# Optimization experiments

Measured on AMD Instinct MI355X. Metric: run time of the kernel, lower is better.

Reference implementation:

```python
import jax, jax.numpy as jnp
import numpy as np

NUM_HEAD = 16
FEAT_DIM = 1024
HEAD_DIM = FEAT_DIM // NUM_HEAD  # 64
MAX_SEQ_LEN = 2048
BATCH = 2


def setup_inputs() -> dict:
    key = jax.random.key(0)
    ks = jax.random.split(key, 6)
    x = jax.random.normal(ks[0], (BATCH, MAX_SEQ_LEN, FEAT_DIM), dtype=jnp.float32)
    # xavier_uniform: limit = sqrt(6/(fan_in+fan_out)); torch Linear weight is [out, in]
    def xavier(k, out_f, in_f):
        lim = float(np.sqrt(6.0 / (in_f + out_f)))
        return jax.random.uniform(k, (out_f, in_f), dtype=jnp.float32, minval=-lim, maxval=lim)
    W1 = xavier(ks[1], HEAD_DIM, HEAD_DIM)          # attn_mlp[0].weight
    b1 = jnp.zeros((HEAD_DIM,), dtype=jnp.float32)
    W2 = xavier(ks[2], MAX_SEQ_LEN, HEAD_DIM)       # attn_mlp[2].weight
    b2 = jnp.zeros((MAX_SEQ_LEN,), dtype=jnp.float32)
    Wv = xavier(ks[3], FEAT_DIM, FEAT_DIM)          # value_linear.weight (no bias)
    Wo = xavier(ks[4], FEAT_DIM, FEAT_DIM)          # output_linear.weight (no bias)
    return {"x": x, "W1": W1, "b1": b1, "W2": W2, "b2": b2, "Wv": Wv, "Wo": Wo}


def _split_head(t):
    b, n, _ = t.shape
    return t.reshape(b, n, NUM_HEAD, HEAD_DIM).transpose(0, 2, 1, 3)  # [b,h,n,d]


def reference(x, W1, b1, W2, b2, Wv, Wo):
    # value projection (dropout is identity in eval / p=0)
    value = x @ Wv.T                                   # [b,n,F]
    vh = _split_head(value)                            # [b,h,n,d]
    xh = _split_head(x)                                # [b,h,n,d]
    # per-head MLP -> dense attention logits [b,h,n,max_seq_len]
    hid = jax.nn.relu(jnp.einsum('bhnd,ed->bhne', xh, W1) + b1)
    logits = jnp.einsum('bhne,me->bhnm', hid, W2) + b2
    attn = jax.nn.softmax(logits, axis=-1)             # [b,h,n,m]
    out_h = jnp.einsum('bhnm,bhmd->bhnd', attn, vh)    # m == seq_len
    b_, h_, n_, d_ = out_h.shape
    out = out_h.transpose(0, 2, 1, 3).reshape(b_, n_, FEAT_DIM)
    return out @ Wo.T
```

## Files before the change

### kernel.cpp

```cpp
#include <hip/hip_runtime.h>
#include <hip/hip_bf16.h>
#include <math.h>
#include <stdint.h>


typedef __attribute__((ext_vector_type(8))) short bf16x8;
typedef __attribute__((ext_vector_type(4))) float f32x4;
typedef __attribute__((ext_vector_type(16))) float f32x16;

#define LOG2E 1.4426950408889634f

__device__ __forceinline__ unsigned short f2bf(float f) {
  union { float f; unsigned u; } v; v.f = f;
  unsigned r = v.u + 0x7FFFu + ((v.u >> 16) & 1u);
  return (unsigned short)(r >> 16);
}

__global__ __launch_bounds__(256) void prep_all(const float* __restrict__ x,
                                                const float* __restrict__ Wv,
                                                const float* __restrict__ Wo,
                                                const float* __restrict__ W2,
                                                const float* __restrict__ W1,
                                                const float* __restrict__ b2,
                                                unsigned short* __restrict__ xb,
                                                unsigned short* __restrict__ wvb,
                                                unsigned short* __restrict__ wob,
                                                unsigned short* __restrict__ w2b,
                                                unsigned short* __restrict__ w1b,
                                                float* __restrict__ b2l) {
  int bid = blockIdx.x;
  if (bid == 2048) {
    int i = threadIdx.x;
#pragma unroll
    for (int t = 0; t < 8; ++t) {
      int k = i * 8 + t;
      b2l[k] = b2[k] * LOG2E;
    }
    return;
  }
  int stride = 2048 * 256;
  for (int q = bid * 256 + threadIdx.x; q < 1606656; q += stride) {
    const float* s; unsigned short* d; int o;
    if (q < 1048576)      { s = x;  d = xb;  o = q; }
    else {
      int q2 = q - 1048576;
      if (q2 < 262144)      { s = Wv; d = wvb; o = q2; }
      else if (q2 < 524288) { s = Wo; d = wob; o = q2 - 262144; }
      else if (q2 < 557056) { s = W2; d = w2b; o = q2 - 524288; }
      else                  { s = W1; d = w1b; o = q2 - 557056; }
    }
    float4 v = *(const float4*)(s + (size_t)o * 4);
    uint2 u;
    u.x = (unsigned)f2bf(v.x) | ((unsigned)f2bf(v.y) << 16);
    u.y = (unsigned)f2bf(v.z) | ((unsigned)f2bf(v.w) << 16);
    *(uint2*)(d + (size_t)o * 4) = u;
  }
}

__device__ __forceinline__ void stage64(const char* g, size_t ldbytes, char* lds,
                                        int w, int lane) {
#pragma unroll
  for (int t = 0; t < 2; ++t) {
    int row  = w * 16 + t * 8 + (lane >> 3);
    int csrc = (lane & 7) ^ (lane >> 3);
    const char* src = g + (size_t)row * ldbytes + (csrc << 4);
    char* dst = lds + ((w * 2 + t) << 10);
    __builtin_amdgcn_global_load_lds((const __attribute__((address_space(1))) void*)src,
                                     (__attribute__((address_space(3))) void*)dst,
                                     16, 0, 0);
  }
}

__device__ __forceinline__ void stage8(const char* g, size_t ldbytes, char* lds_,
                                       int w, int lane) {
  int row  = w * 8 + (lane >> 3);
  int csrc = (lane & 7) ^ (lane >> 3);
  const char* src = g + (size_t)row * ldbytes + (csrc << 4);
  char* dst = lds_ + (w << 10);
  __builtin_amdgcn_global_load_lds((const __attribute__((address_space(1))) void*)src,
                                   (__attribute__((address_space(3))) void*)dst,
                                   16, 0, 0);
}

__device__ __forceinline__ bf16x8 rdfrag32(const char* lds, int row, int chunk) {
  int c = chunk ^ (row & 7);
  return *(const bf16x8*)(lds + row * 128 + (c << 4));
}

__device__ __forceinline__ f32x16 loadb16(const float* p) {
  f32x16 r;
#pragma unroll
  for (int qd = 0; qd < 4; ++qd) {
    float4 v = *(const float4*)(p + qd * 8);
    r[qd * 4 + 0] = v.x; r[qd * 4 + 1] = v.y; r[qd * 4 + 2] = v.z; r[qd * 4 + 3] = v.w;
  }
  return r;
}

__device__ __forceinline__ bf16x8 pk_swap(float r0, float r1, float r2, float r3,
                                          float r4, float r5, float r6, float r7) {
  unsigned a, b, c, d;
  asm("v_cvt_pk_bf16_f32 %0, %1, %2" : "=v"(a) : "v"(r0), "v"(r1));
  asm("v_cvt_pk_bf16_f32 %0, %1, %2" : "=v"(b) : "v"(r4), "v"(r5));
  asm("v_cvt_pk_bf16_f32 %0, %1, %2" : "=v"(c) : "v"(r2), "v"(r3));
  asm("v_cvt_pk_bf16_f32 %0, %1, %2" : "=v"(d) : "v"(r6), "v"(r7));
  asm("v_permlane32_swap_b32 %0, %1" : "+v"(a), "+v"(b));
  asm("v_permlane32_swap_b32 %0, %1" : "+v"(c), "+v"(d));
  union { unsigned u[4]; bf16x8 v; } r;
  r.u[0] = a; r.u[1] = c; r.u[2] = b; r.u[3] = d;
  return r.v;
}

template<int MODE>
__global__ __launch_bounds__(256) void gemm12864(const unsigned short* __restrict__ A,
                                                 const unsigned short* __restrict__ B,
                                                 void* __restrict__ C, int K) {
  __shared__ __attribute__((aligned(16))) char As[2][16384];
  __shared__ __attribute__((aligned(16))) char Bs[2][8192];
  int tid = threadIdx.x, w = tid >> 6, lane = tid & 63;
  int l31 = lane & 31, hi = lane >> 5;
  int wr = w >> 1, wc = w & 1;
  int bm = blockIdx.x, bn = blockIdx.y;
  const char* Ab = (const char*)A + (size_t)bm * 128 * (K * 2);
  const char* Bb = (const char*)B + (size_t)bn * 64 * (K * 2);
  size_t ld = (size_t)K * 2;

  f32x16 acc0 = {}, acc1 = {};
  stage64(Ab, ld, As[0], w, lane);
  stage64(Ab + 64 * ld, ld, As[0] + 8192, w, lane);
  stage64(Bb, ld, Bs[0], w, lane);
  __syncthreads();

  int nst = K >> 6;
  for (int kk = 0; kk < nst; ++kk) {
    int cur = kk & 1;
    if (kk + 1 < nst) {
      const char* An = Ab + (size_t)(kk + 1) * 128;
      const char* Bn = Bb + (size_t)(kk + 1) * 128;
      stage64(An, ld, As[cur ^ 1], w, lane);
      stage64(An + 64 * ld, ld, As[cur ^ 1] + 8192, w, lane);
      stage64(Bn, ld, Bs[cur ^ 1], w, lane);
    }
    __builtin_amdgcn_s_setprio(1);
#pragma unroll
    for (int ks = 0; ks < 4; ++ks) {
      bf16x8 a0 = rdfrag32(As[cur], wr * 64 + l31, ks * 2 + hi);
      bf16x8 a1 = rdfrag32(As[cur], wr * 64 + 32 + l31, ks * 2 + hi);
      bf16x8 b0 = rdfrag32(Bs[cur], wc * 32 + l31, ks * 2 + hi);
      acc0 = __builtin_amdgcn_mfma_f32_32x32x16_bf16(a0, b0, acc0, 0, 0, 0);
      acc1 = __builtin_amdgcn_mfma_f32_32x32x16_bf16(a1, b0, acc1, 0, 0, 0);
    }
    __builtin_amdgcn_s_setprio(0);
    __syncthreads();
  }

  if (MODE == 0) {
    unsigned short* vt = (unsigned short*)C;
    int d = wc * 32 + l31;
#pragma unroll
    for (int i = 0; i < 2; ++i) {
      f32x16 a = i ? acc1 : acc0;
      int rowb = bm * 128 + wr * 64 + i * 32;
#pragma unroll
      for (int qd = 0; qd < 4; ++qd) {
        int m0 = rowb + qd * 8 + hi * 4;
        int bb = m0 >> 11, n = m0 & 2047;
        int r0 = qd * 4;
        uint2 u;
        u.x = (unsigned)f2bf(a[r0]) | ((unsigned)f2bf(a[r0 + 1]) << 16);
        u.y = (unsigned)f2bf(a[r0 + 2]) | ((unsigned)f2bf(a[r0 + 3]) << 16);
        *(uint2*)(vt + ((size_t)((bb * 16 + bn) * 64 + d)) * 2048 + n) = u;
      }
    }
  } else {
    float* Cf = (float*)C;
    int rb = bm * 128 + wr * 64, cb = bn * 64 + wc * 32;
#pragma unroll
    for (int r = 0; r < 16; ++r) {
      int row = (r & 3) + 8 * (r >> 2) + 4 * hi;
      Cf[(size_t)(rb + row) * 1024 + cb + l31]      = acc0[r];
      Cf[(size_t)(rb + 32 + row) * 1024 + cb + l31] = acc1[r];
    }
  }
}

__global__ __launch_bounds__(512, 2) void flash_kernel(const unsigned short* __restrict__ xb,
                                                       const unsigned short* __restrict__ w1b,
                                                       const float* __restrict__ b1,
                                                       const unsigned short* __restrict__ w2b,
                                                       const float* __restrict__ b2l,
                                                       const unsigned short* __restrict__ vt,
                                                       unsigned short* __restrict__ aout) {
  __shared__ __attribute__((aligned(16))) char lds[73728];
  int tid = threadIdx.x, w = tid >> 6, lane = tid & 63;
  int wq = w & 3, grp = w >> 2;
  int l31 = lane & 31, hi = lane >> 5;
  int f = blockIdx.x;
  int swz = ((f & 7) << 6) | (f >> 3);
  int qt = swz & 15, bh = swz >> 4;
  int b = bh >> 4, h = bh & 15;

  const char* px = (const char*)(xb + ((size_t)(b * 2048 + qt * 128)) * 1024 + h * 64);
  stage8(px, 2048, lds, w, lane);
  stage8(px + (size_t)64 * 2048, 2048, lds + 8192, w, lane);
  stage8((const char*)w1b, 128, lds + 32768, w, lane);
  {
    const char* src = (const char*)b2l + (w << 10) + (lane << 4);
    char* dst = lds + 65536 + (w << 10);
    __builtin_amdgcn_global_load_lds((const __attribute__((address_space(1))) void*)src,
                                     (__attribute__((address_space(3))) void*)dst,
                                     16, 0, 0);
  }
  __syncthreads();

  f32x16 h0 = loadb16(b1 + hi * 4);
  f32x16 h1 = loadb16(b1 + 32 + hi * 4);
  {
    const char* xt = lds + (wq >> 1) * 8192;
    int xr = (wq & 1) * 32 + l31;
#pragma unroll
    for (int ks = 0; ks < 4; ++ks) {
      bf16x8 xf = rdfrag32(xt, xr, ks * 2 + hi);
      bf16x8 wf0 = rdfrag32(lds + 32768, l31, ks * 2 + hi);
      h0 = __builtin_amdgcn_mfma_f32_32x32x16_bf16(wf0, xf, h0, 0, 0, 0);
      bf16x8 wf1 = rdfrag32(lds + 32768, 32 + l31, ks * 2 + hi);
      h1 = __builtin_amdgcn_mfma_f32_32x32x16_bf16(wf1, xf, h1, 0, 0, 0);
    }
  }
#pragma unroll
  for (int i = 0; i < 16; ++i) {
    h0[i] = fmaxf(h0[i], 0.f) * LOG2E;
    h1[i] = fmaxf(h1[i], 0.f) * LOG2E;
  }
  bf16x8 qb[4];
  qb[0] = pk_swap(h0[0], h0[1], h0[2], h0[3], h0[4], h0[5], h0[6], h0[7]);
  qb[1] = pk_swap(h0[8], h0[9], h0[10], h0[11], h0[12], h0[13], h0[14], h0[15]);
  qb[2] = pk_swap(h1[0], h1[1], h1[2], h1[3], h1[4], h1[5], h1[6], h1[7]);
  qb[3] = pk_swap(h1[8], h1[9], h1[10], h1[11], h1[12], h1[13], h1[14], h1[15]);
  __syncthreads();

  const char* vtb = (const char*)vt + (size_t)bh * 64 * 4096;
#pragma unroll
  for (int t = 0; t < 4; ++t) {
    stage8((const char*)w2b + (size_t)t * 8192, 128, lds + t * 8192, w, lane);
    stage8(vtb + (size_t)t * 128, 4096, lds + 32768 + t * 8192, w, lane);
  }
  bf16x8 ones;
#pragma unroll
  for (int i = 0; i < 8; ++i) ones[i] = (short)0x3F80;
  f32x16 oA = {}, oB = {}, Lac = {};
  const float* bl = (const float*)(lds + 65536);
  __syncthreads();

  for (int s = 0; s < 16; ++s) {
    int mt = 2 * s + grp;
    const char* Kc = lds + (mt & 3) * 8192;
    const char* Vc = lds + 32768 + (mt & 3) * 8192;

    if (s >= 1 && s <= 14) {
      int t0 = 2 * s + 2, t1 = 2 * s + 3;
      stage8((const char*)w2b + (size_t)t0 * 8192, 128, lds + (t0 & 3) * 8192, w, lane);
      stage8(vtb + (size_t)t0 * 128, 4096, lds + 32768 + (t0 & 3) * 8192, w, lane);
      stage8((const char*)w2b + (size_t)t1 * 8192, 128, lds + (t1 & 3) * 8192, w, lane);
      stage8(vtb + (size_t)t1 * 128, 4096, lds + 32768 + (t1 & 3) * 8192, w, lane);
    }

    f32x16 s0, s1;
#pragma unroll
    for (int qd = 0; qd < 4; ++qd) {
      f32x4 p0 = *(const f32x4*)(bl + mt * 64 + qd * 8 + hi * 4);
      f32x4 p1 = *(const f32x4*)(bl + mt * 64 + 32 + qd * 8 + hi * 4);
#pragma unroll
      for (int j = 0; j < 4; ++j) {
        s0[qd * 4 + j] = p0[j];
        s1[qd * 4 + j] = p1[j];
      }
    }
    __builtin_amdgcn_s_setprio(1);
#pragma unroll
    for (int kt = 0; kt < 4; ++kt) {
      bf16x8 kf0 = rdfrag32(Kc, l31, kt * 2 + hi);
      s0 = __builtin_amdgcn_mfma_f32_32x32x16_bf16(kf0, qb[kt], s0, 0, 0, 0);
      bf16x8 kf1 = rdfrag32(Kc, 32 + l31, kt * 2 + hi);
      s1 = __builtin_amdgcn_mfma_f32_32x32x16_bf16(kf1, qb[kt], s1, 0, 0, 0);
    }
    __builtin_amdgcn_s_setprio(0);
#pragma unroll
    for (int i = 0; i < 16; ++i) {
      float t0, t1;
      asm("v_exp_f32 %0, %1" : "=v"(t0) : "v"(s0[i]));
      asm("v_exp_f32 %0, %1" : "=v"(t1) : "v"(s1[i]));
      s0[i] = t0; s1[i] = t1;
    }
    bf16x8 pa0 = pk_swap(s0[0], s0[1], s0[2], s0[3], s0[4], s0[5], s0[6], s0[7]);
    bf16x8 pa1 = pk_swap(s0[8], s0[9], s0[10], s0[11], s0[12], s0[13], s0[14], s0[15]);
    bf16x8 pa2 = pk_swap(s1[0], s1[1], s1[2], s1[3], s1[4], s1[5], s1[6], s1[7]);
    bf16x8 pa3 = pk_swap(s1[8], s1[9], s1[10], s1[11], s1[12], s1[13], s1[14], s1[15]);
    __builtin_amdgcn_s_setprio(1);
    Lac = __builtin_amdgcn_mfma_f32_32x32x16_bf16(pa0, ones, Lac, 0, 0, 0);
    Lac = __builtin_amdgcn_mfma_f32_32x32x16_bf16(pa1, ones, Lac, 0, 0, 0);
    Lac = __builtin_amdgcn_mfma_f32_32x32x16_bf16(pa2, ones, Lac, 0, 0, 0);
    Lac = __builtin_amdgcn_mfma_f32_32x32x16_bf16(pa3, ones, Lac, 0, 0, 0);
    {
      bf16x8 vf;
      vf = rdfrag32(Vc, l31, 0 + hi);
      oA = __builtin_amdgcn_mfma_f32_32x32x16_bf16(pa0, vf, oA, 0, 0, 0);
      vf = rdfrag32(Vc, 32 + l31, 0 + hi);
      oB = __builtin_amdgcn_mfma_f32_32x32x16_bf16(pa0, vf, oB, 0, 0, 0);
      vf = rdfrag32(Vc, l31, 2 + hi);
      oA = __builtin_amdgcn_mfma_f32_32x32x16_bf16(pa1, vf, oA, 0, 0, 0);
      vf = rdfrag32(Vc, 32 + l31, 2 + hi);
      oB = __builtin_amdgcn_mfma_f32_32x32x16_bf16(pa1, vf, oB, 0, 0, 0);
      vf = rdfrag32(Vc, l31, 4 + hi);
      oA = __builtin_amdgcn_mfma_f32_32x32x16_bf16(pa2, vf, oA, 0, 0, 0);
      vf = rdfrag32(Vc, 32 + l31, 4 + hi);
      oB = __builtin_amdgcn_mfma_f32_32x32x16_bf16(pa2, vf, oB, 0, 0, 0);
      vf = rdfrag32(Vc, l31, 6 + hi);
      oA = __builtin_amdgcn_mfma_f32_32x32x16_bf16(pa3, vf, oA, 0, 0, 0);
      vf = rdfrag32(Vc, 32 + l31, 6 + hi);
      oB = __builtin_amdgcn_mfma_f32_32x32x16_bf16(pa3, vf, oB, 0, 0, 0);
    }
    __builtin_amdgcn_s_setprio(0);
    __syncthreads();
  }

  float* comb = (float*)lds;
  if (grp == 1) {
    float* cb = comb + (wq * 64 + lane) * 52;
#pragma unroll
    for (int i = 0; i < 4; ++i) {
      *(float4*)(cb + i * 4)      = make_float4(oA[i*4], oA[i*4+1], oA[i*4+2], oA[i*4+3]);
      *(float4*)(cb + 16 + i * 4) = make_float4(oB[i*4], oB[i*4+1], oB[i*4+2], oB[i*4+3]);
      *(float4*)(cb + 32 + i * 4) = make_float4(Lac[i*4], Lac[i*4+1], Lac[i*4+2], Lac[i*4+3]);
    }
  }
  __syncthreads();
  if (grp == 0) {
    float* cb = comb + (wq * 64 + lane) * 52;
#pragma unroll
    for (int i = 0; i < 4; ++i) {
      float4 a = *(const float4*)(cb + i * 4);
      float4 bq = *(const float4*)(cb + 16 + i * 4);
      float4 c = *(const float4*)(cb + 32 + i * 4);
      oA[i*4] += a.x;  oA[i*4+1] += a.y;  oA[i*4+2] += a.z;  oA[i*4+3] += a.w;
      oB[i*4] += bq.x; oB[i*4+1] += bq.y; oB[i*4+2] += bq.z; oB[i*4+3] += bq.w;
      Lac[i*4] += c.x; Lac[i*4+1] += c.y; Lac[i*4+2] += c.z; Lac[i*4+3] += c.w;
    }
    int nb = qt * 128 + wq * 32;
#pragma unroll
    for (int r = 0; r < 16; ++r) {
      float iv = 1.f / Lac[r];
      int ql = (r & 3) + 8 * (r >> 2) + 4 * hi;
      size_t off = ((size_t)(b * 2048 + nb + ql)) * 1024 + h * 64 + l31;
      aout[off]      = f2bf(oA[r] * iv);
      aout[off + 32] = f2bf(oB[r] * iv);
    }
  }
}

extern "C" void kernel_launch(void* const* d_in, const int* in_sizes, int n_in,
                              void* d_out, int out_size, void* d_ws, size_t ws_size,
                              hipStream_t stream) {
  (void)in_sizes; (void)n_in; (void)out_size; (void)ws_size;
  const float* x  = (const float*)d_in[0];
  const float* W1 = (const float*)d_in[1];
  const float* b1 = (const float*)d_in[2];
  const float* W2 = (const float*)d_in[3];
  const float* b2 = (const float*)d_in[4];
  const float* Wv = (const float*)d_in[5];
  const float* Wo = (const float*)d_in[6];
  float* out = (float*)d_out;

  char* ws = (char*)d_ws;
  unsigned short* xb   = (unsigned short*)(ws);
  unsigned short* wvb  = (unsigned short*)(ws +  8388608);
  unsigned short* wob  = (unsigned short*)(ws + 10485760);
  unsigned short* w2b  = (unsigned short*)(ws + 12582912);
  unsigned short* w1b  = (unsigned short*)(ws + 12845056);
  float*          b2l  = (float*)         (ws + 12853248);
  unsigned short* vt   = (unsigned short*)(ws + 21233664);
  unsigned short* aout = (unsigned short*)(ws + 29622272);

  prep_all<<<2049, 256, 0, stream>>>(x, Wv, Wo, W2, W1, b2,
                                     xb, wvb, wob, w2b, w1b, b2l);

  gemm12864<0><<<dim3(32, 16), 256, 0, stream>>>(xb, wvb, (void*)vt, 1024);
  flash_kernel<<<512, 512, 0, stream>>>(xb, w1b, b1, w2b, b2l, vt, aout);
  gemm12864<1><<<dim3(32, 16), 256, 0, stream>>>(aout, wob, (void*)out, 1024);
}
```

Before: 92.28 us.

## Fold exp(b2) into V and row-sum weights, switch bf16 to fp16 MFMA

The bias b2 is moved out of the logits: exp(b2) is folded into the value projection output and into the B operand of the row-sum MFMA. This removes the per-tile bias LDS load and staging and shrinks LDS. All operands switch from bf16 to fp16 with round-toward-zero packing. This risks overflow or precision issues if values exceed the fp16 range, and it assumes b2 is bounded.

```diff
diff --git a/kernel.cpp b/kernel.cpp
--- a/kernel.cpp
+++ b/kernel.cpp
@@ -4,16 +4,17 @@
 #include <stdint.h>
 
 
-typedef __attribute__((ext_vector_type(8))) short bf16x8;
+typedef __attribute__((ext_vector_type(8))) _Float16 f16x8;
+typedef __attribute__((ext_vector_type(2))) __fp16 h2;
 typedef __attribute__((ext_vector_type(4))) float f32x4;
 typedef __attribute__((ext_vector_type(16))) float f32x16;
 
 #define LOG2E 1.4426950408889634f
 
-__device__ __forceinline__ unsigned short f2bf(float f) {
-  union { float f; unsigned u; } v; v.f = f;
-  unsigned r = v.u + 0x7FFFu + ((v.u >> 16) & 1u);
-  return (unsigned short)(r >> 16);
+__device__ __forceinline__ unsigned short f2h(float f) {
+  union { _Float16 h; unsigned short u; } v;
+  v.h = (_Float16)f;
+  return v.u;
 }
 
 __global__ __launch_bounds__(256) void prep_all(const float* __restrict__ x,
@@ -27,14 +28,17 @@
                                                 unsigned short* __restrict__ wob,
                                                 unsigned short* __restrict__ w2b,
                                                 unsigned short* __restrict__ w1b,
-                                                float* __restrict__ b2l) {
+                                                float* __restrict__ eb2f,
+                                                unsigned short* __restrict__ ebb) {
   int bid = blockIdx.x;
   if (bid == 2048) {
     int i = threadIdx.x;
 #pragma unroll
     for (int t = 0; t < 8; ++t) {
       int k = i * 8 + t;
-      b2l[k] = b2[k] * LOG2E;
+      float e = __expf(b2[k]);
+      eb2f[k] = e;
+      ebb[k] = f2h(e);
     }
     return;
   }
@@ -51,8 +55,8 @@
     }
     float4 v = *(const float4*)(s + (size_t)o * 4);
     uint2 u;
-    u.x = (unsigned)f2bf(v.x) | ((unsigned)f2bf(v.y) << 16);
-    u.y = (unsigned)f2bf(v.z) | ((unsigned)f2bf(v.w) << 16);
+    u.x = (unsigned)f2h(v.x) | ((unsigned)f2h(v.y) << 16);
+    u.y = (unsigned)f2h(v.z) | ((unsigned)f2h(v.w) << 16);
     *(uint2*)(d + (size_t)o * 4) = u;
   }
 }
@@ -82,9 +86,9 @@
                                    16, 0, 0);
 }
 
-__device__ __forceinline__ bf16x8 rdfrag32(const char* lds, int row, int chunk) {
+__device__ __forceinline__ f16x8 rdfrag32(const char* lds, int row, int chunk) {
   int c = chunk ^ (row & 7);
-  return *(const bf16x8*)(lds + row * 128 + (c << 4));
+  return *(const f16x8*)(lds + row * 128 + (c << 4));
 }
 
 __device__ __forceinline__ f32x16 loadb16(const float* p) {
@@ -97,24 +101,25 @@
   return r;
 }
 
-__device__ __forceinline__ bf16x8 pk_swap(float r0, float r1, float r2, float r3,
-                                          float r4, float r5, float r6, float r7) {
-  unsigned a, b, c, d;
-  asm("v_cvt_pk_bf16_f32 %0, %1, %2" : "=v"(a) : "v"(r0), "v"(r1));
-  asm("v_cvt_pk_bf16_f32 %0, %1, %2" : "=v"(b) : "v"(r4), "v"(r5));
-  asm("v_cvt_pk_bf16_f32 %0, %1, %2" : "=v"(c) : "v"(r2), "v"(r3));
-  asm("v_cvt_pk_bf16_f32 %0, %1, %2" : "=v"(d) : "v"(r6), "v"(r7));
-  asm("v_permlane32_swap_b32 %0, %1" : "+v"(a), "+v"(b));
-  asm("v_permlane32_swap_b32 %0, %1" : "+v"(c), "+v"(d));
-  union { unsigned u[4]; bf16x8 v; } r;
-  r.u[0] = a; r.u[1] = c; r.u[2] = b; r.u[3] = d;
+__device__ __forceinline__ f16x8 pk_swap(float r0, float r1, float r2, float r3,
+                                         float r4, float r5, float r6, float r7) {
+  union { h2 h; unsigned u; } a, b, c, d;
+  a.h = __builtin_amdgcn_cvt_pkrtz(r0, r1);
+  b.h = __builtin_amdgcn_cvt_pkrtz(r4, r5);
+  c.h = __builtin_amdgcn_cvt_pkrtz(r2, r3);
+  d.h = __builtin_amdgcn_cvt_pkrtz(r6, r7);
+  asm("v_permlane32_swap_b32 %0, %1" : "+v"(a.u), "+v"(b.u));
+  asm("v_permlane32_swap_b32 %0, %1" : "+v"(c.u), "+v"(d.u));
+  union { unsigned u[4]; f16x8 v; } r;
+  r.u[0] = a.u; r.u[1] = c.u; r.u[2] = b.u; r.u[3] = d.u;
   return r.v;
 }
 
 template<int MODE>
 __global__ __launch_bounds__(256) void gemm12864(const unsigned short* __restrict__ A,
                                                  const unsigned short* __restrict__ B,
-                                                 void* __restrict__ C, int K) {
+                                                 void* __restrict__ C,
+                                                 const float* __restrict__ eb2f, int K) {
   __shared__ __attribute__((aligned(16))) char As[2][16384];
   __shared__ __attribute__((aligned(16))) char Bs[2][8192];
   int tid = threadIdx.x, w = tid >> 6, lane = tid & 63;
@@ -144,11 +149,11 @@
     __builtin_amdgcn_s_setprio(1);
 #pragma unroll
     for (int ks = 0; ks < 4; ++ks) {
-      bf16x8 a0 = rdfrag32(As[cur], wr * 64 + l31, ks * 2 + hi);
-      bf16x8 a1 = rdfrag32(As[cur], wr * 64 + 32 + l31, ks * 2 + hi);
-      bf16x8 b0 = rdfrag32(Bs[cur], wc * 32 + l31, ks * 2 + hi);
-      acc0 = __builtin_amdgcn_mfma_f32_32x32x16_bf16(a0, b0, acc0, 0, 0, 0);
-      acc1 = __builtin_amdgcn_mfma_f32_32x32x16_bf16(a1, b0, acc1, 0, 0, 0);
+      f16x8 a0 = rdfrag32(As[cur], wr * 64 + l31, ks * 2 + hi);
+      f16x8 a1 = rdfrag32(As[cur], wr * 64 + 32 + l31, ks * 2 + hi);
+      f16x8 b0 = rdfrag32(Bs[cur], wc * 32 + l31, ks * 2 + hi);
+      acc0 = __builtin_amdgcn_mfma_f32_32x32x16_f16(a0, b0, acc0, 0, 0, 0);
+      acc1 = __builtin_amdgcn_mfma_f32_32x32x16_f16(a1, b0, acc1, 0, 0, 0);
     }
     __builtin_amdgcn_s_setprio(0);
     __syncthreads();
@@ -164,11 +169,12 @@
 #pragma unroll
       for (int qd = 0; qd < 4; ++qd) {
         int m0 = rowb + qd * 8 + hi * 4;
+        float4 e4 = *(const float4*)(eb2f + (m0 & 2047));
         int bb = m0 >> 11, n = m0 & 2047;
         int r0 = qd * 4;
         uint2 u;
-        u.x = (unsigned)f2bf(a[r0]) | ((unsigned)f2bf(a[r0 + 1]) << 16);
-        u.y = (unsigned)f2bf(a[r0 + 2]) | ((unsigned)f2bf(a[r0 + 3]) << 16);
+        u.x = (unsigned)f2h(a[r0] * e4.x) | ((unsigned)f2h(a[r0 + 1] * e4.y) << 16);
+        u.y = (unsigned)f2h(a[r0 + 2] * e4.z) | ((unsigned)f2h(a[r0 + 3] * e4.w) << 16);
         *(uint2*)(vt + ((size_t)((bb * 16 + bn) * 64 + d)) * 2048 + n) = u;
       }
     }
@@ -188,10 +194,10 @@
                                                        const unsigned short* __restrict__ w1b,
                                                        const float* __restrict__ b1,
                                                        const unsigned short* __restrict__ w2b,
-                                                       const float* __restrict__ b2l,
+                                                       const unsigned short* __restrict__ ebb,
                                                        const unsigned short* __restrict__ vt,
                                                        unsigned short* __restrict__ aout) {
-  __shared__ __attribute__((aligned(16))) char lds[73728];
+  __shared__ __attribute__((aligned(16))) char lds[65536];
   int tid = threadIdx.x, w = tid >> 6, lane = tid & 63;
   int wq = w & 3, grp = w >> 2;
   int l31 = lane & 31, hi = lane >> 5;
@@ -204,13 +210,6 @@
   stage8(px, 2048, lds, w, lane);
   stage8(px + (size_t)64 * 2048, 2048, lds + 8192, w, lane);
   stage8((const char*)w1b, 128, lds + 32768, w, lane);
-  {
-    const char* src = (const char*)b2l + (w << 10) + (lane << 4);
-    char* dst = lds + 65536 + (w << 10);
-    __builtin_amdgcn_global_load_lds((const __attribute__((address_space(1))) void*)src,
-                                     (__attribute__((address_space(3))) void*)dst,
-                                     16, 0, 0);
-  }
   __syncthreads();
 
   f32x16 h0 = loadb16(b1 + hi * 4);
@@ -220,11 +219,11 @@
     int xr = (wq & 1) * 32 + l31;
 #pragma unroll
     for (int ks = 0; ks < 4; ++ks) {
-      bf16x8 xf = rdfrag32(xt, xr, ks * 2 + hi);
-      bf16x8 wf0 = rdfrag32(lds + 32768, l31, ks * 2 + hi);
-      h0 = __builtin_amdgcn_mfma_f32_32x32x16_bf16(wf0, xf, h0, 0, 0, 0);
-      bf16x8 wf1 = rdfrag32(lds + 32768, 32 + l31, ks * 2 + hi);
-      h1 = __builtin_amdgcn_mfma_f32_32x32x16_bf16(wf1, xf, h1, 0, 0, 0);
+      f16x8 xf = rdfrag32(xt, xr, ks * 2 + hi);
+      f16x8 wf0 = rdfrag32(lds + 32768, l31, ks * 2 + hi);
+      h0 = __builtin_amdgcn_mfma_f32_32x32x16_f16(wf0, xf, h0, 0, 0, 0);
+      f16x8 wf1 = rdfrag32(lds + 32768, 32 + l31, ks * 2 + hi);
+      h1 = __builtin_amdgcn_mfma_f32_32x32x16_f16(wf1, xf, h1, 0, 0, 0);
     }
   }
 #pragma unroll
@@ -232,7 +231,7 @@
     h0[i] = fmaxf(h0[i], 0.f) * LOG2E;
     h1[i] = fmaxf(h1[i], 0.f) * LOG2E;
   }
-  bf16x8 qb[4];
+  f16x8 qb[4];
   qb[0] = pk_swap(h0[0], h0[1], h0[2], h0[3], h0[4], h0[5], h0[6], h0[7]);
   qb[1] = pk_swap(h0[8], h0[9], h0[10], h0[11], h0[12], h0[13], h0[14], h0[15]);
   qb[2] = pk_swap(h1[0], h1[1], h1[2], h1[3], h1[4], h1[5], h1[6], h1[7]);
@@ -245,11 +244,8 @@
     stage8((const char*)w2b + (size_t)t * 8192, 128, lds + t * 8192, w, lane);
     stage8(vtb + (size_t)t * 128, 4096, lds + 32768 + t * 8192, w, lane);
   }
-  bf16x8 ones;
-#pragma unroll
-  for (int i = 0; i < 8; ++i) ones[i] = (short)0x3F80;
+  const f32x16 zro = {};
   f32x16 oA = {}, oB = {}, Lac = {};
-  const float* bl = (const float*)(lds + 65536);
   __syncthreads();
 
   for (int s = 0; s < 16; ++s) {
@@ -265,24 +261,19 @@
       stage8(vtb + (size_t)t1 * 128, 4096, lds + 32768 + (t1 & 3) * 8192, w, lane);
     }
 
-    f32x16 s0, s1;
-#pragma unroll
-    for (int qd = 0; qd < 4; ++qd) {
-      f32x4 p0 = *(const f32x4*)(bl + mt * 64 + qd * 8 + hi * 4);
-      f32x4 p1 = *(const f32x4*)(bl + mt * 64 + 32 + qd * 8 + hi * 4);
-#pragma unroll
-      for (int j = 0; j < 4; ++j) {
-        s0[qd * 4 + j] = p0[j];
-        s1[qd * 4 + j] = p1[j];
-      }
-    }
+    f16x8 ebf0 = *(const f16x8*)(ebb + mt * 64 + hi * 8);
+    f16x8 ebf1 = *(const f16x8*)(ebb + mt * 64 + 16 + hi * 8);
+    f16x8 ebf2 = *(const f16x8*)(ebb + mt * 64 + 32 + hi * 8);
+    f16x8 ebf3 = *(const f16x8*)(ebb + mt * 64 + 48 + hi * 8);
+
+    f32x16 s0 = zro, s1 = zro;
     __builtin_amdgcn_s_setprio(1);
 #pragma unroll
     for (int kt = 0; kt < 4; ++kt) {
-      bf16x8 kf0 = rdfrag32(Kc, l31, kt * 2 + hi);
-      s0 = __builtin_amdgcn_mfma_f32_32x32x16_bf16(kf0, qb[kt], s0, 0, 0, 0);
-      bf16x8 kf1 = rdfrag32(Kc, 32 + l31, kt * 2 + hi);
-      s1 = __builtin_amdgcn_mfma_f32_32x32x16_bf16(kf1, qb[kt], s1, 0, 0, 0);
+      f16x8 kf0 = rdfrag32(Kc, l31, kt * 2 + hi);
+      s0 = __builtin_amdgcn_mfma_f32_32x32x16_f16(kf0, qb[kt], s0, 0, 0, 0);
+      f16x8 kf1 = rdfrag32(Kc, 32 + l31, kt * 2 + hi);
+      s1 = __builtin_amdgcn_mfma_f32_32x32x16_f16(kf1, qb[kt], s1, 0, 0, 0);
     }
     __builtin_amdgcn_s_setprio(0);
 #pragma unroll
@@ -292,33 +283,33 @@
       asm("v_exp_f32 %0, %1" : "=v"(t1) : "v"(s1[i]));
       s0[i] = t0; s1[i] = t1;
     }
-    bf16x8 pa0 = pk_swap(s0[0], s0[1], s0[2], s0[3], s0[4], s0[5], s0[6], s0[7]);
-    bf16x8 pa1 = pk_swap(s0[8], s0[9], s0[10], s0[11], s0[12], s0[13], s0[14], s0[15]);
-    bf16x8 pa2 = pk_swap(s1[0], s1[1], s1[2], s1[3], s1[4], s1[5], s1[6], s1[7]);
-    bf16x8 pa3 = pk_swap(s1[8], s1[9], s1[10], s1[11], s1[12], s1[13], s1[14], s1[15]);
+    f16x8 pa0 = pk_swap(s0[0], s0[1], s0[2], s0[3], s0[4], s0[5], s0[6], s0[7]);
+    f16x8 pa1 = pk_swap(s0[8], s0[9], s0[10], s0[11], s0[12], s0[13], s0[14], s0[15]);
+    f16x8 pa2 = pk_swap(s1[0], s1[1], s1[2], s1[3], s1[4], s1[5], s1[6], s1[7]);
+    f16x8 pa3 = pk_swap(s1[8], s1[9], s1[10], s1[11], s1[12], s1[13], s1[14], s1[15]);
     __builtin_amdgcn_s_setprio(1);
-    Lac = __builtin_amdgcn_mfma_f32_32x32x16_bf16(pa0, ones, Lac, 0, 0, 0);
-    Lac = __builtin_amdgcn_mfma_f32_32x32x16_bf16(pa1, ones, Lac, 0, 0, 0);
-    Lac = __builtin_amdgcn_mfma_f32_32x32x16_bf16(pa2, ones, Lac, 0, 0, 0);
-    Lac = __builtin_amdgcn_mfma_f32_32x32x16_bf16(pa3, ones, Lac, 0, 0, 0);
+    Lac = __builtin_amdgcn_mfma_f32_32x32x16_f16(pa0, ebf0, Lac, 0, 0, 0);
+    Lac = __builtin_amdgcn_mfma_f32_32x32x16_f16(pa1, ebf1, Lac, 0, 0, 0);
+    Lac = __builtin_amdgcn_mfma_f32_32x32x16_f16(pa2, ebf2, Lac, 0, 0, 0);
+    Lac = __builtin_amdgcn_mfma_f32_32x32x16_f16(pa3, ebf3, Lac, 0, 0, 0);
     {
-      bf16x8 vf;
+      f16x8 vf;
       vf = rdfrag32(Vc, l31, 0 + hi);
-      oA = __builtin_amdgcn_mfma_f32_32x32x16_bf16(pa0, vf, oA, 0, 0, 0);
+      oA = __builtin_amdgcn_mfma_f32_32x32x16_f16(pa0, vf, oA, 0, 0, 0);
       vf = rdfrag32(Vc, 32 + l31, 0 + hi);
-      oB = __builtin_amdgcn_mfma_f32_32x32x16_bf16(pa0, vf, oB, 0, 0, 0);
+      oB = __builtin_amdgcn_mfma_f32_32x32x16_f16(pa0, vf, oB, 0, 0, 0);
       vf = rdfrag32(Vc, l31, 2 + hi);
-      oA = __builtin_amdgcn_mfma_f32_32x32x16_bf16(pa1, vf, oA, 0, 0, 0);
+      oA = __builtin_amdgcn_mfma_f32_32x32x16_f16(pa1, vf, oA, 0, 0, 0);
       vf = rdfrag32(Vc, 32 + l31, 2 + hi);
-      oB = __builtin_amdgcn_mfma_f32_32x32x16_bf16(pa1, vf, oB, 0, 0, 0);
+      oB = __builtin_amdgcn_mfma_f32_32x32x16_f16(pa1, vf, oB, 0, 0, 0);
       vf = rdfrag32(Vc, l31, 4 + hi);
-      oA = __builtin_amdgcn_mfma_f32_32x32x16_bf16(pa2, vf, oA, 0, 0, 0);
+      oA = __builtin_amdgcn_mfma_f32_32x32x16_f16(pa2, vf, oA, 0, 0, 0);
       vf = rdfrag32(Vc, 32 + l31, 4 + hi);
-      oB = __builtin_amdgcn_mfma_f32_32x32x16_bf16(pa2, vf, oB, 0, 0, 0);
+      oB = __builtin_amdgcn_mfma_f32_32x32x16_f16(pa2, vf, oB, 0, 0, 0);
       vf = rdfrag32(Vc, l31, 6 + hi);
-      oA = __builtin_amdgcn_mfma_f32_32x32x16_bf16(pa3, vf, oA, 0, 0, 0);
+      oA = __builtin_amdgcn_mfma_f32_32x32x16_f16(pa3, vf, oA, 0, 0, 0);
       vf = rdfrag32(Vc, 32 + l31, 6 + hi);
-      oB = __builtin_amdgcn_mfma_f32_32x32x16_bf16(pa3, vf, oB, 0, 0, 0);
+      oB = __builtin_amdgcn_mfma_f32_32x32x16_f16(pa3, vf, oB, 0, 0, 0);
     }
     __builtin_amdgcn_s_setprio(0);
     __syncthreads();
@@ -352,8 +343,8 @@
       float iv = 1.f / Lac[r];
       int ql = (r & 3) + 8 * (r >> 2) + 4 * hi;
       size_t off = ((size_t)(b * 2048 + nb + ql)) * 1024 + h * 64 + l31;
-      aout[off]      = f2bf(oA[r] * iv);
-      aout[off + 32] = f2bf(oB[r] * iv);
+      aout[off]      = f2h(oA[r] * iv);
+      aout[off + 32] = f2h(oB[r] * iv);
     }
   }
 }
@@ -377,14 +368,15 @@
   unsigned short* wob  = (unsigned short*)(ws + 10485760);
   unsigned short* w2b  = (unsigned short*)(ws + 12582912);
   unsigned short* w1b  = (unsigned short*)(ws + 12845056);
-  float*          b2l  = (float*)         (ws + 12853248);
+  float*          eb2f = (float*)         (ws + 12853248);
+  unsigned short* ebb  = (unsigned short*)(ws + 12861440);
   unsigned short* vt   = (unsigned short*)(ws + 21233664);
   unsigned short* aout = (unsigned short*)(ws + 29622272);
 
   prep_all<<<2049, 256, 0, stream>>>(x, Wv, Wo, W2, W1, b2,
-                                     xb, wvb, wob, w2b, w1b, b2l);
-
-  gemm12864<0><<<dim3(32, 16), 256, 0, stream>>>(xb, wvb, (void*)vt, 1024);
-  flash_kernel<<<512, 512, 0, stream>>>(xb, w1b, b1, w2b, b2l, vt, aout);
-  gemm12864<1><<<dim3(32, 16), 256, 0, stream>>>(aout, wob, (void*)out, 1024);
-}
+                                     xb, wvb, wob, w2b, w1b, eb2f, ebb);
+
+  gemm12864<0><<<dim3(32, 16), 256, 0, stream>>>(xb, wvb, (void*)vt, eb2f, 1024);
+  flash_kernel<<<512, 512, 0, stream>>>(xb, w1b, b1, w2b, ebb, vt, aout);
+  gemm12864<1><<<dim3(32, 16), 256, 0, stream>>>(aout, wob, (void*)out, eb2f, 1024);
+}
```

Result: slower. 99.22 us (+7.5%).
